# Kernel optimization log

Hardware: AMD Instinct MI355X
Metric: run time of the kernel (lower is better)

The kernel has to match this reference:

```python
import jax, jax.numpy as jnp
import numpy as np

N_NODES = 50000
N_EDGES = 800000
IN_DIM = 1200   # latent_size * num_heads
OUT_DIM = 300
NEG_SLOPE = 0.2  # PyG GATConv default


def setup_inputs() -> dict:
    key = jax.random.key(0)
    k1, k2, k3, k4, k5 = jax.random.split(key, 5)
    z = jax.random.normal(k1, (N_NODES, IN_DIM), dtype=jnp.float32)
    edge_index = jax.random.randint(k2, (2, N_EDGES), 0, N_NODES, dtype=jnp.int64)
    # GATConv params (heads=1): lin weight [out, in], attention vectors [out], bias [out]
    W = jax.random.normal(k3, (OUT_DIM, IN_DIM), dtype=jnp.float32) * (1.0 / np.sqrt(IN_DIM))
    att_src = jax.random.normal(k4, (OUT_DIM,), dtype=jnp.float32) * 0.1
    att_dst = jax.random.normal(k5, (OUT_DIM,), dtype=jnp.float32) * 0.1
    bias = jnp.zeros((OUT_DIM,), dtype=jnp.float32)
    return {"z": z, "edge_index": edge_index, "W": W,
            "att_src": att_src, "att_dst": att_dst, "bias": bias}


def reference(z, edge_index, W, att_src, att_dst, bias):
    N = z.shape[0]
    # Linear projection (no bias on lin in GATConv; bias added after aggregation)
    x = z @ W.T                                   # [N, OUT_DIM]
    # add self-loops (GATConv default add_self_loops=True)
    loop = jnp.arange(N, dtype=edge_index.dtype)
    src = jnp.concatenate([edge_index[0], loop])  # message source j
    dst = jnp.concatenate([edge_index[1], loop])  # message target i
    # per-node attention logits
    a_src = x @ att_src                           # [N]
    a_dst = x @ att_dst                           # [N]
    # per-edge score, softmax over incoming edges of each target node
    e = jax.nn.leaky_relu(a_src[src] + a_dst[dst], negative_slope=NEG_SLOPE)  # [E+N]
    e_max = jax.ops.segment_max(e, dst, num_segments=N)   # every node has a self-loop
    ex = jnp.exp(e - e_max[dst])
    denom = jax.ops.segment_sum(ex, dst, num_segments=N)
    alpha = ex / denom[dst]                       # [E+N]
    # weighted aggregation (scatter-add over targets)
    out = jax.ops.segment_sum(alpha[:, None] * x[src], dst, num_segments=N)
    return out + bias
```

## Files before the change

### kernel.cpp

```cpp
#include <hip/hip_runtime.h>

#define N_NODES 50000
#define N_EDGES 800000
#define IN_DIM  1200
#define OUT_DIM 300
#define XBS     304
#define NSLOTS  (N_EDGES + N_NODES)

typedef __attribute__((ext_vector_type(8))) short short8;
typedef __attribute__((ext_vector_type(4))) float f32x4;

__device__ __forceinline__ short f2bf(float f) {
  unsigned u = __builtin_bit_cast(unsigned, f);
  u += 0x7fffu + ((u >> 16) & 1u);
  return (short)(u >> 16);
}
__device__ __forceinline__ float bf2f(unsigned short h) {
  return __builtin_bit_cast(float, (unsigned)h << 16);
}
__device__ __forceinline__ float lrelu(float v) { return v > 0.f ? v : 0.2f * v; }

__device__ __forceinline__ float wredMaxF(float v) {
  #pragma unroll
  for (int o = 32; o > 0; o >>= 1) v = fmaxf(v, __shfl_xor(v, o));
  return v;
}
__device__ __forceinline__ float wredSumF(float v) {
  #pragma unroll
  for (int o = 32; o > 0; o >>= 1) v += __shfl_xor(v, o);
  return v;
}

__global__ __launch_bounds__(256) void wconv(const float* __restrict__ W,
                                             unsigned short* __restrict__ Wb) {
  int f = blockIdx.x * 256 + threadIdx.x;
  if (f >= 304 * IN_DIM / 8) return;
  int n = (f * 8) / IN_DIM, c = (f * 8) % IN_DIM;
  short8 v = {0,0,0,0,0,0,0,0};
  if (n < OUT_DIM) {
    const float4* p = reinterpret_cast<const float4*>(W + (size_t)n * IN_DIM + c);
    float4 f0 = p[0], f1 = p[1];
    v[0]=f2bf(f0.x); v[1]=f2bf(f0.y); v[2]=f2bf(f0.z); v[3]=f2bf(f0.w);
    v[4]=f2bf(f1.x); v[5]=f2bf(f1.y); v[6]=f2bf(f1.z); v[7]=f2bf(f1.w);
  }
  *reinterpret_cast<short8*>(&Wb[(size_t)n * IN_DIM + c]) = v;
}

__global__ __launch_bounds__(256, 2) void gemm_x(const float* __restrict__ z,
                                                 const unsigned short* __restrict__ Wb,
                                                 const float* __restrict__ att_s,
                                                 const float* __restrict__ att_d,
                                                 unsigned short* __restrict__ xb,
                                                 float* __restrict__ a_s,
                                                 float* __restrict__ a_d) {
  __shared__ unsigned short As[128 * 40];
  __shared__ unsigned short Bs[304 * 40];

  const int tid  = threadIdx.x;
  const int lane = tid & 63;
  const int wid  = tid >> 6;
  const int m0   = blockIdx.x * 128;
  const int lr   = lane & 15;
  const int lg   = lane >> 4;
  const int lk   = lg * 8;

  f32x4 zero4 = {0.f, 0.f, 0.f, 0.f};
  f32x4 acc[2][19];
  #pragma unroll
  for (int h = 0; h < 2; ++h)
    #pragma unroll
    for (int t = 0; t < 19; ++t) acc[h][t] = zero4;

  const int ar = tid >> 1;
  const int ac = (tid & 1) * 16;
  const int bn = tid >> 2;
  const int bc = (tid & 3) * 8;

  for (int kt = 0; kt < 38; ++kt) {
    const int k0 = kt * 32;
    {
      int m = m0 + ar, k = k0 + ac;
      short8 v0 = {0,0,0,0,0,0,0,0}, v1 = v0;
      if (m < N_NODES && k + 15 < IN_DIM) {
        const float4* p = reinterpret_cast<const float4*>(z + (size_t)m * IN_DIM + k);
        float4 f0 = p[0], f1 = p[1], f2 = p[2], f3 = p[3];
        v0[0]=f2bf(f0.x); v0[1]=f2bf(f0.y); v0[2]=f2bf(f0.z); v0[3]=f2bf(f0.w);
        v0[4]=f2bf(f1.x); v0[5]=f2bf(f1.y); v0[6]=f2bf(f1.z); v0[7]=f2bf(f1.w);
        v1[0]=f2bf(f2.x); v1[1]=f2bf(f2.y); v1[2]=f2bf(f2.z); v1[3]=f2bf(f2.w);
        v1[4]=f2bf(f3.x); v1[5]=f2bf(f3.y); v1[6]=f2bf(f3.z); v1[7]=f2bf(f3.w);
      }
      *reinterpret_cast<short8*>(&As[ar * 40 + ac]) = v0;
      *reinterpret_cast<short8*>(&As[ar * 40 + ac + 8]) = v1;
    }
    #pragma unroll
    for (int p5 = 0; p5 < 5; ++p5) {
      int n = bn + 64 * p5;
      if (n < 304) {
        int k = k0 + bc;
        short8 v = {0,0,0,0,0,0,0,0};
        if (k + 7 < IN_DIM)
          v = *reinterpret_cast<const short8*>(&Wb[(size_t)n * IN_DIM + k]);
        *reinterpret_cast<short8*>(&Bs[n * 40 + bc]) = v;
      }
    }
    __syncthreads();

    short8 af0 = *reinterpret_cast<const short8*>(&As[(32 * wid + lr) * 40 + lk]);
    short8 af1 = *reinterpret_cast<const short8*>(&As[(32 * wid + 16 + lr) * 40 + lk]);
    #pragma unroll
    for (int t = 0; t < 19; ++t) {
      short8 bf = *reinterpret_cast<const short8*>(&Bs[(16 * t + lr) * 40 + lk]);
      acc[0][t] = __builtin_amdgcn_mfma_f32_16x16x32_bf16(af0, bf, acc[0][t], 0, 0, 0);
      acc[1][t] = __builtin_amdgcn_mfma_f32_16x16x32_bf16(af1, bf, acc[1][t], 0, 0, 0);
    }
    __syncthreads();
  }

  #pragma unroll
  for (int h = 0; h < 2; ++h) {
    const int rbase = m0 + 32 * wid + 16 * h + 4 * lg;
    float ps[4] = {0.f,0.f,0.f,0.f}, pd[4] = {0.f,0.f,0.f,0.f};
    #pragma unroll
    for (int t = 0; t < 19; ++t) {
      int c = 16 * t + lr;
      if (c < OUT_DIM) {
        float vs = att_s[c], vd = att_d[c];
        #pragma unroll
        for (int j = 0; j < 4; ++j) {
          float val = acc[h][t][j];
          int r = rbase + j;
          if (r < N_NODES) xb[(size_t)r * XBS + c] = (unsigned short)f2bf(val);
          ps[j] += val * vs;
          pd[j] += val * vd;
        }
      }
    }
    #pragma unroll
    for (int j = 0; j < 4; ++j) {
      #pragma unroll
      for (int o = 8; o > 0; o >>= 1) {
        ps[j] += __shfl_xor(ps[j], o);
        pd[j] += __shfl_xor(pd[j], o);
      }
    }
    if (lr == 0) {
      #pragma unroll
      for (int j = 0; j < 4; ++j) {
        int r = rbase + j;
        if (r < N_NODES) { a_s[r] = ps[j]; a_d[r] = pd[j]; }
      }
    }
  }
}

__global__ void hist(const int* __restrict__ ei, int* __restrict__ deg) {
  int e = blockIdx.x * blockDim.x + threadIdx.x;
  if (e < N_EDGES) {
    unsigned dst = (unsigned)ei[N_EDGES + e];
    if (dst < N_NODES) atomicAdd(&deg[dst], 1);
  }
}

#define SCAN_B 1024
#define NBLK   49

__global__ __launch_bounds__(SCAN_B) void scan1(const int* __restrict__ deg,
                                                int* __restrict__ bsum) {
  int i = blockIdx.x * SCAN_B + threadIdx.x;
  int v = (i < N_NODES) ? deg[i] + 1 : 0;
  #pragma unroll
  for (int o = 32; o > 0; o >>= 1) v += __shfl_xor(v, o);
  __shared__ int wt[16];
  if ((threadIdx.x & 63) == 0) wt[threadIdx.x >> 6] = v;
  __syncthreads();
  if (threadIdx.x == 0) {
    int t = 0;
    #pragma unroll
    for (int w = 0; w < 16; ++w) t += wt[w];
    bsum[blockIdx.x] = t;
  }
}

__global__ void scan2(const int* __restrict__ bsum, int* __restrict__ bex,
                      int* __restrict__ offs) {
  int l = threadIdx.x;
  int v = (l < NBLK) ? bsum[l] : 0;
  int incl = v;
  #pragma unroll
  for (int off = 1; off < 64; off <<= 1) {
    int u = __shfl_up(incl, off);
    if (l >= off) incl += u;
  }
  if (l < NBLK) bex[l] = incl - v;
  if (l == NBLK - 1) offs[N_NODES] = incl;
}

__global__ __launch_bounds__(SCAN_B) void scan3(const int* __restrict__ deg,
                                                const int* __restrict__ bex,
                                                int* __restrict__ offs,
                                                int* __restrict__ cursor) {
  int tid = threadIdx.x;
  int i = blockIdx.x * SCAN_B + tid;
  int lane = tid & 63, wid = tid >> 6;
  int v = (i < N_NODES) ? deg[i] + 1 : 0;
  int incl = v;
  #pragma unroll
  for (int off = 1; off < 64; off <<= 1) {
    int u = __shfl_up(incl, off);
    if (lane >= off) incl += u;
  }
  __shared__ int wt[16];
  if (lane == 63) wt[wid] = incl;
  __syncthreads();
  if (tid < 16) {
    int t = wt[tid];
    int sc = t;
    #pragma unroll
    for (int off = 1; off < 16; off <<= 1) {
      int u = __shfl_up(sc, off);
      if (tid >= off) sc += u;
    }
    wt[tid] = sc - t;
  }
  __syncthreads();
  int excl = incl - v + wt[wid] + bex[blockIdx.x];
  if (i < N_NODES) { offs[i] = excl; cursor[i] = excl; }
}

__global__ void fill(const int* __restrict__ ei, int* __restrict__ cursor,
                     int* __restrict__ srcs) {
  int e = blockIdx.x * blockDim.x + threadIdx.x;
  if (e < N_EDGES) {
    unsigned dst = (unsigned)ei[N_EDGES + e];
    unsigned src = (unsigned)ei[e];
    if (dst < N_NODES && src < N_NODES) {
      int pos = atomicAdd(&cursor[dst], 1);
      srcs[pos] = (int)src;
    }
  }
}

__global__ __launch_bounds__(256) void weights(const float* __restrict__ a_s,
                                               const float* __restrict__ a_d,
                                               const int* __restrict__ offs,
                                               const int* __restrict__ srcs,
                                               int2* __restrict__ packed) {
  int node = blockIdx.x * 4 + (threadIdx.x >> 6);
  if (node >= N_NODES) return;
  int lane = threadIdx.x & 63;
  int beg = offs[node], end = offs[node + 1];
  int ne = end - 1 - beg;
  float adi = a_d[node];
  float eself = lrelu(a_s[node] + adi);

  float m = eself;
  for (int k = lane; k < ne; k += 64)
    m = fmaxf(m, lrelu(a_s[srcs[beg + k]] + adi));
  m = wredMaxF(m);

  float s = 0.f;
  for (int k = lane; k < ne; k += 64)
    s += expf(lrelu(a_s[srcs[beg + k]] + adi) - m);
  s = wredSumF(s) + expf(eself - m);
  float inv = 1.0f / s;

  for (int k = lane; k < ne; k += 64) {
    int sj = srcs[beg + k];
    float w = expf(lrelu(a_s[sj] + adi) - m) * inv;
    packed[beg + k] = make_int2(sj, __float_as_int(w));
  }
  if (lane == 0)
    packed[end - 1] = make_int2(node, __float_as_int(expf(eself - m) * inv));
}

__global__ __launch_bounds__(256) void aggregate(const unsigned short* __restrict__ xb,
                                                 const int2* __restrict__ packed,
                                                 const int* __restrict__ offs,
                                                 const float* __restrict__ bias,
                                                 float* __restrict__ out) {
  unsigned wi = blockIdx.x * 256u + threadIdx.x;
  if (wi >= (unsigned)N_NODES * 75u) return;
  unsigned node = wi / 75u;
  unsigned cc = wi - node * 75u;

  int beg = offs[node], end = offs[node + 1];
  const unsigned short* xcol = xb + 4u * cc;

  float4 acc = {0.f, 0.f, 0.f, 0.f};
  for (int k = beg; k < end; ++k) {
    int2 pw = packed[k];
    float w = __builtin_bit_cast(float, pw.y);
    ushort4 xv = *reinterpret_cast<const ushort4*>(xcol + (size_t)pw.x * XBS);
    acc.x += w * bf2f(xv.x);
    acc.y += w * bf2f(xv.y);
    acc.z += w * bf2f(xv.z);
    acc.w += w * bf2f(xv.w);
  }
  const float4 b = *reinterpret_cast<const float4*>(bias + 4u * cc);
  float4 o = {acc.x + b.x, acc.y + b.y, acc.z + b.z, acc.w + b.w};
  *reinterpret_cast<float4*>(out + (size_t)node * OUT_DIM + 4u * cc) = o;
}

extern "C" void kernel_launch(void* const* d_in, const int* in_sizes, int n_in,
                              void* d_out, int out_size, void* d_ws, size_t ws_size,
                              hipStream_t stream) {
  const float* z     = (const float*)d_in[0];
  const int*   ei    = (const int*)d_in[1];
  const float* W     = (const float*)d_in[2];
  const float* att_s = (const float*)d_in[3];
  const float* att_d = (const float*)d_in[4];
  const float* bias  = (const float*)d_in[5];
  float* out = (float*)d_out;

  char* ws = (char*)d_ws;
  size_t off = 0;
  unsigned short* xb   = (unsigned short*)(ws + off); off += (size_t)N_NODES * XBS * 2;
  unsigned short* Wb   = (unsigned short*)(ws + off); off += (size_t)304 * IN_DIM * 2;
  float* a_s  = (float*)(ws + off); off += 50048 * 4;
  float* a_d  = (float*)(ws + off); off += 50048 * 4;
  int*   deg  = (int*)(ws + off);   off += 50048 * 4;
  int*   offs = (int*)(ws + off);   off += 50056 * 4;
  int*   cur  = (int*)(ws + off);   off += 50048 * 4;
  int*   bsum = (int*)(ws + off);   off += 64 * 4;
  int*   bex  = (int*)(ws + off);   off += 64 * 4;
  int*   srcs = (int*)(ws + off);   off += (size_t)NSLOTS * 4;
  int2*  pck  = (int2*)(ws + off);  off += (size_t)NSLOTS * 8;

  hipMemsetAsync(deg, 0, N_NODES * 4, stream);

  wconv<<<(304 * IN_DIM / 8 + 255) / 256, 256, 0, stream>>>(W, Wb);
  gemm_x<<<(N_NODES + 127) / 128, 256, 0, stream>>>(z, Wb, att_s, att_d, xb, a_s, a_d);
  hist<<<(N_EDGES + 255) / 256, 256, 0, stream>>>(ei, deg);
  scan1<<<NBLK, SCAN_B, 0, stream>>>(deg, bsum);
  scan2<<<1, 64, 0, stream>>>(bsum, bex, offs);
  scan3<<<NBLK, SCAN_B, 0, stream>>>(deg, bex, offs, cur);
  fill<<<(N_EDGES + 255) / 256, 256, 0, stream>>>(ei, cur, srcs);
  weights<<<(N_NODES + 3) / 4, 256, 0, stream>>>(a_s, a_d, offs, srcs, pck);
  aggregate<<<((unsigned)N_NODES * 75u + 255) / 256, 256, 0, stream>>>(xb, pck, offs, bias, out);
}
```

Baseline: 364.3 us.

## Restructure projection GEMM tiling and widen per-thread aggregation columns

The projection GEMM moves from 128-row tiles with both operands staged in LDS to 96-row tiles. Only z is staged in LDS, with an XOR swizzle and register prefetch of the next K-tile. Each wave reads its 80-column slice of padded bf16 W directly from global memory, and the attention-logit reduction now goes across waves through LDS. The aggregate kernel gives each thread 20 columns instead of 4, so each thread reads the packed edge entry once per 20 columns instead of once per 4. The cost is higher register pressure and fewer threads, which lowers the parallelism available to hide gather latency.

```diff
diff --git a/kernel.cpp b/kernel.cpp
--- a/kernel.cpp
+++ b/kernel.cpp
@@ -3,9 +3,13 @@
 #define N_NODES 50000
 #define N_EDGES 800000
 #define IN_DIM  1200
+#define KP      1216
 #define OUT_DIM 300
+#define BNP     320
 #define XBS     304
 #define NSLOTS  (N_EDGES + N_NODES)
+#define BM      96
+#define GRID_M  ((N_NODES + BM - 1) / BM)
 
 typedef __attribute__((ext_vector_type(8))) short short8;
 typedef __attribute__((ext_vector_type(4))) float f32x4;
@@ -34,16 +38,16 @@
 __global__ __launch_bounds__(256) void wconv(const float* __restrict__ W,
                                              unsigned short* __restrict__ Wb) {
   int f = blockIdx.x * 256 + threadIdx.x;
-  if (f >= 304 * IN_DIM / 8) return;
-  int n = (f * 8) / IN_DIM, c = (f * 8) % IN_DIM;
+  if (f >= BNP * KP / 8) return;
+  int n = (f * 8) / KP, c = (f * 8) % KP;
   short8 v = {0,0,0,0,0,0,0,0};
-  if (n < OUT_DIM) {
+  if (n < OUT_DIM && c < IN_DIM) {
     const float4* p = reinterpret_cast<const float4*>(W + (size_t)n * IN_DIM + c);
     float4 f0 = p[0], f1 = p[1];
     v[0]=f2bf(f0.x); v[1]=f2bf(f0.y); v[2]=f2bf(f0.z); v[3]=f2bf(f0.w);
     v[4]=f2bf(f1.x); v[5]=f2bf(f1.y); v[6]=f2bf(f1.z); v[7]=f2bf(f1.w);
   }
-  *reinterpret_cast<short8*>(&Wb[(size_t)n * IN_DIM + c]) = v;
+  *reinterpret_cast<short8*>(&Wb[(size_t)n * KP + c]) = v;
 }
 
 __global__ __launch_bounds__(256, 2) void gemm_x(const float* __restrict__ z,
@@ -53,103 +57,131 @@
                                                  unsigned short* __restrict__ xb,
                                                  float* __restrict__ a_s,
                                                  float* __restrict__ a_d) {
-  __shared__ unsigned short As[128 * 40];
-  __shared__ unsigned short Bs[304 * 40];
+  __shared__ unsigned short As[BM * 64];
 
   const int tid  = threadIdx.x;
   const int lane = tid & 63;
   const int wid  = tid >> 6;
-  const int m0   = blockIdx.x * 128;
   const int lr   = lane & 15;
   const int lg   = lane >> 4;
-  const int lk   = lg * 8;
+  const int m0   = blockIdx.x * BM;
 
   f32x4 zero4 = {0.f, 0.f, 0.f, 0.f};
-  f32x4 acc[2][19];
-  #pragma unroll
-  for (int h = 0; h < 2; ++h)
-    #pragma unroll
-    for (int t = 0; t < 19; ++t) acc[h][t] = zero4;
-
-  const int ar = tid >> 1;
-  const int ac = (tid & 1) * 16;
-  const int bn = tid >> 2;
-  const int bc = (tid & 3) * 8;
-
-  for (int kt = 0; kt < 38; ++kt) {
-    const int k0 = kt * 32;
-    {
-      int m = m0 + ar, k = k0 + ac;
-      short8 v0 = {0,0,0,0,0,0,0,0}, v1 = v0;
-      if (m < N_NODES && k + 15 < IN_DIM) {
-        const float4* p = reinterpret_cast<const float4*>(z + (size_t)m * IN_DIM + k);
-        float4 f0 = p[0], f1 = p[1], f2 = p[2], f3 = p[3];
-        v0[0]=f2bf(f0.x); v0[1]=f2bf(f0.y); v0[2]=f2bf(f0.z); v0[3]=f2bf(f0.w);
-        v0[4]=f2bf(f1.x); v0[5]=f2bf(f1.y); v0[6]=f2bf(f1.z); v0[7]=f2bf(f1.w);
-        v1[0]=f2bf(f2.x); v1[1]=f2bf(f2.y); v1[2]=f2bf(f2.z); v1[3]=f2bf(f2.w);
-        v1[4]=f2bf(f3.x); v1[5]=f2bf(f3.y); v1[6]=f2bf(f3.z); v1[7]=f2bf(f3.w);
+  const float4 fz4 = make_float4(0.f, 0.f, 0.f, 0.f);
+  f32x4 acc[6][5];
+  #pragma unroll
+  for (int mf = 0; mf < 6; ++mf)
+    #pragma unroll
+    for (int nj = 0; nj < 5; ++nj) acc[mf][nj] = zero4;
+
+  const unsigned short* bp = Wb + (size_t)(80 * wid + lr) * KP + lg * 8;
+
+  float4 st[3][2];
+  const int srow[3] = { (tid + 0)   >> 3, (tid + 256) >> 3, (tid + 512) >> 3 };
+  const int sch [3] = { (tid + 0)   & 7,  (tid + 256) & 7,  (tid + 512) & 7  };
+
+  #define LOADST(KT)                                                          \
+    _Pragma("unroll")                                                         \
+    for (int j = 0; j < 3; ++j) {                                             \
+      int m = m0 + srow[j], k = (KT) * 64 + sch[j] * 8;                       \
+      if (m < N_NODES && k < IN_DIM) {                                        \
+        const float4* p = reinterpret_cast<const float4*>(z + (size_t)m * IN_DIM + k); \
+        st[j][0] = p[0]; st[j][1] = p[1];                                     \
+      } else { st[j][0] = fz4; st[j][1] = fz4; }                              \
+    }
+
+  LOADST(0);
+
+  for (int kt = 0; kt < 19; ++kt) {
+    __syncthreads();
+    #pragma unroll
+    for (int j = 0; j < 3; ++j) {
+      short8 v;
+      v[0]=f2bf(st[j][0].x); v[1]=f2bf(st[j][0].y); v[2]=f2bf(st[j][0].z); v[3]=f2bf(st[j][0].w);
+      v[4]=f2bf(st[j][1].x); v[5]=f2bf(st[j][1].y); v[6]=f2bf(st[j][1].z); v[7]=f2bf(st[j][1].w);
+      int c2 = sch[j] ^ (srow[j] & 7);
+      *reinterpret_cast<short8*>(&As[srow[j] * 64 + c2 * 8]) = v;
+    }
+    __syncthreads();
+    if (kt < 18) { LOADST(kt + 1) }
+
+    const unsigned short* bpk = bp + kt * 64;
+    short8 bfr[5][2];
+    #pragma unroll
+    for (int nj = 0; nj < 5; ++nj) {
+      bfr[nj][0] = *reinterpret_cast<const short8*>(bpk + (size_t)nj * 16 * KP);
+      bfr[nj][1] = *reinterpret_cast<const short8*>(bpk + (size_t)nj * 16 * KP + 32);
+    }
+
+    const int sw = lr & 7;
+    #pragma unroll
+    for (int mf = 0; mf < 6; ++mf) {
+      int arow = mf * 16 + lr;
+      short8 a0 = *reinterpret_cast<const short8*>(&As[arow * 64 + ((lg    ) ^ sw) * 8]);
+      short8 a1 = *reinterpret_cast<const short8*>(&As[arow * 64 + ((4 + lg) ^ sw) * 8]);
+      #pragma unroll
+      for (int nj = 0; nj < 5; ++nj) {
+        acc[mf][nj] = __builtin_amdgcn_mfma_f32_16x16x32_bf16(a0, bfr[nj][0], acc[mf][nj], 0, 0, 0);
+        acc[mf][nj] = __builtin_amdgcn_mfma_f32_16x16x32_bf16(a1, bfr[nj][1], acc[mf][nj], 0, 0, 0);
       }
-      *reinterpret_cast<short8*>(&As[ar * 40 + ac]) = v0;
-      *reinterpret_cast<short8*>(&As[ar * 40 + ac + 8]) = v1;
-    }
-    #pragma unroll
-    for (int p5 = 0; p5 < 5; ++p5) {
-      int n = bn + 64 * p5;
-      if (n < 304) {
-        int k = k0 + bc;
-        short8 v = {0,0,0,0,0,0,0,0};
-        if (k + 7 < IN_DIM)
-          v = *reinterpret_cast<const short8*>(&Wb[(size_t)n * IN_DIM + k]);
-        *reinterpret_cast<short8*>(&Bs[n * 40 + bc]) = v;
+    }
+  }
+  #undef LOADST
+
+  __syncthreads();
+  float* red = reinterpret_cast<float*>(As);
+
+  float vs[5], vd[5];
+  #pragma unroll
+  for (int nj = 0; nj < 5; ++nj) {
+    int c = 80 * wid + 16 * nj + lr;
+    bool cv = c < OUT_DIM;
+    vs[nj] = cv ? att_s[c] : 0.f;
+    vd[nj] = cv ? att_d[c] : 0.f;
+  }
+
+  #pragma unroll
+  for (int mf = 0; mf < 6; ++mf) {
+    float ps[4] = {0.f,0.f,0.f,0.f}, pd[4] = {0.f,0.f,0.f,0.f};
+    #pragma unroll
+    for (int nj = 0; nj < 5; ++nj) {
+      int c = 80 * wid + 16 * nj + lr;
+      bool cv = c < OUT_DIM;
+      #pragma unroll
+      for (int jj = 0; jj < 4; ++jj) {
+        float val = acc[mf][nj][jj];
+        int r = m0 + 16 * mf + 4 * lg + jj;
+        if (cv && r < N_NODES) xb[(size_t)r * XBS + c] = (unsigned short)f2bf(val);
+        ps[jj] += val * vs[nj];
+        pd[jj] += val * vd[nj];
       }
     }
-    __syncthreads();
-
-    short8 af0 = *reinterpret_cast<const short8*>(&As[(32 * wid + lr) * 40 + lk]);
-    short8 af1 = *reinterpret_cast<const short8*>(&As[(32 * wid + 16 + lr) * 40 + lk]);
-    #pragma unroll
-    for (int t = 0; t < 19; ++t) {
-      short8 bf = *reinterpret_cast<const short8*>(&Bs[(16 * t + lr) * 40 + lk]);
-      acc[0][t] = __builtin_amdgcn_mfma_f32_16x16x32_bf16(af0, bf, acc[0][t], 0, 0, 0);
-      acc[1][t] = __builtin_amdgcn_mfma_f32_16x16x32_bf16(af1, bf, acc[1][t], 0, 0, 0);
-    }
-    __syncthreads();
-  }
-
-  #pragma unroll
-  for (int h = 0; h < 2; ++h) {
-    const int rbase = m0 + 32 * wid + 16 * h + 4 * lg;
-    float ps[4] = {0.f,0.f,0.f,0.f}, pd[4] = {0.f,0.f,0.f,0.f};
-    #pragma unroll
-    for (int t = 0; t < 19; ++t) {
-      int c = 16 * t + lr;
-      if (c < OUT_DIM) {
-        float vs = att_s[c], vd = att_d[c];
-        #pragma unroll
-        for (int j = 0; j < 4; ++j) {
-          float val = acc[h][t][j];
-          int r = rbase + j;
-          if (r < N_NODES) xb[(size_t)r * XBS + c] = (unsigned short)f2bf(val);
-          ps[j] += val * vs;
-          pd[j] += val * vd;
-        }
-      }
-    }
-    #pragma unroll
-    for (int j = 0; j < 4; ++j) {
+    #pragma unroll
+    for (int jj = 0; jj < 4; ++jj) {
       #pragma unroll
       for (int o = 8; o > 0; o >>= 1) {
-        ps[j] += __shfl_xor(ps[j], o);
-        pd[j] += __shfl_xor(pd[j], o);
+        ps[jj] += __shfl_xor(ps[jj], o);
+        pd[jj] += __shfl_xor(pd[jj], o);
       }
     }
     if (lr == 0) {
       #pragma unroll
-      for (int j = 0; j < 4; ++j) {
-        int r = rbase + j;
-        if (r < N_NODES) { a_s[r] = ps[j]; a_d[r] = pd[j]; }
+      for (int jj = 0; jj < 4; ++jj) {
+        int rr = 16 * mf + 4 * lg + jj;
+        red[wid * 96 + rr]       = ps[jj];
+        red[384 + wid * 96 + rr] = pd[jj];
       }
     }
+  }
+  __syncthreads();
+  if (tid < 96) {
+    int r = m0 + tid;
+    if (r < N_NODES)
+      a_s[r] = red[tid] + red[96 + tid] + red[192 + tid] + red[288 + tid];
+  } else if (tid < 192) {
+    int t = tid - 96, r = m0 + t;
+    if (r < N_NODES)
+      a_d[r] = red[384 + t] + red[384 + 96 + t] + red[384 + 192 + t] + red[384 + 288 + t];
   }
 }
 
@@ -273,32 +305,45 @@
     packed[end - 1] = make_int2(node, __float_as_int(expf(eself - m) * inv));
 }
 
+#define CCH 15
 __global__ __launch_bounds__(256) void aggregate(const unsigned short* __restrict__ xb,
                                                  const int2* __restrict__ packed,
                                                  const int* __restrict__ offs,
                                                  const float* __restrict__ bias,
                                                  float* __restrict__ out) {
   unsigned wi = blockIdx.x * 256u + threadIdx.x;
-  if (wi >= (unsigned)N_NODES * 75u) return;
-  unsigned node = wi / 75u;
-  unsigned cc = wi - node * 75u;
+  if (wi >= (unsigned)N_NODES * CCH) return;
+  unsigned node = wi / CCH;
+  unsigned cc = wi - node * CCH;
 
   int beg = offs[node], end = offs[node + 1];
-  const unsigned short* xcol = xb + 4u * cc;
-
-  float4 acc = {0.f, 0.f, 0.f, 0.f};
+  const unsigned short* xcol = xb + 20u * cc;
+
+  float acc[20];
+  #pragma unroll
+  for (int q = 0; q < 20; ++q) acc[q] = 0.f;
+
   for (int k = beg; k < end; ++k) {
     int2 pw = packed[k];
     float w = __builtin_bit_cast(float, pw.y);
-    ushort4 xv = *reinterpret_cast<const ushort4*>(xcol + (size_t)pw.x * XBS);
-    acc.x += w * bf2f(xv.x);
-    acc.y += w * bf2f(xv.y);
-    acc.z += w * bf2f(xv.z);
-    acc.w += w * bf2f(xv.w);
-  }
-  const float4 b = *reinterpret_cast<const float4*>(bias + 4u * cc);
-  float4 o = {acc.x + b.x, acc.y + b.y, acc.z + b.z, acc.w + b.w};
-  *reinterpret_cast<float4*>(out + (size_t)node * OUT_DIM + 4u * cc) = o;
+    const unsigned short* xr = xcol + (size_t)pw.x * XBS;
+    #pragma unroll
+    for (int q = 0; q < 5; ++q) {
+      ushort4 xv = *reinterpret_cast<const ushort4*>(xr + 4 * q);
+      acc[4*q+0] += w * bf2f(xv.x);
+      acc[4*q+1] += w * bf2f(xv.y);
+      acc[4*q+2] += w * bf2f(xv.z);
+      acc[4*q+3] += w * bf2f(xv.w);
+    }
+  }
+  float* op = out + (size_t)node * OUT_DIM + 20u * cc;
+  const float* bp = bias + 20u * cc;
+  #pragma unroll
+  for (int q = 0; q < 5; ++q) {
+    float4 b = *reinterpret_cast<const float4*>(bp + 4 * q);
+    float4 o = {acc[4*q] + b.x, acc[4*q+1] + b.y, acc[4*q+2] + b.z, acc[4*q+3] + b.w};
+    *reinterpret_cast<float4*>(op + 4 * q) = o;
+  }
 }
 
 extern "C" void kernel_launch(void* const* d_in, const int* in_sizes, int n_in,
@@ -314,8 +359,8 @@
 
   char* ws = (char*)d_ws;
   size_t off = 0;
-  unsigned short* xb   = (unsigned short*)(ws + off); off += (size_t)N_NODES * XBS * 2;
-  unsigned short* Wb   = (unsigned short*)(ws + off); off += (size_t)304 * IN_DIM * 2;
+  unsigned short* xb = (unsigned short*)(ws + off); off += (size_t)N_NODES * XBS * 2;
+  unsigned short* Wb = (unsigned short*)(ws + off); off += (size_t)BNP * KP * 2;
   float* a_s  = (float*)(ws + off); off += 50048 * 4;
   float* a_d  = (float*)(ws + off); off += 50048 * 4;
   int*   deg  = (int*)(ws + off);   off += 50048 * 4;
@@ -326,15 +371,15 @@
   int*   srcs = (int*)(ws + off);   off += (size_t)NSLOTS * 4;
   int2*  pck  = (int2*)(ws + off);  off += (size_t)NSLOTS * 8;
 
-  hipMemsetAsync(deg, 0, N_NODES * 4, stream);
-
-  wconv<<<(304 * IN_DIM / 8 + 255) / 256, 256, 0, stream>>>(W, Wb);
-  gemm_x<<<(N_NODES + 127) / 128, 256, 0, stream>>>(z, Wb, att_s, att_d, xb, a_s, a_d);
+  (void)hipMemsetAsync(deg, 0, N_NODES * 4, stream);
+
+  wconv<<<(BNP * KP / 8 + 255) / 256, 256, 0, stream>>>(W, Wb);
+  gemm_x<<<GRID_M, 256, 0, stream>>>(z, Wb, att_s, att_d, xb, a_s, a_d);
   hist<<<(N_EDGES + 255) / 256, 256, 0, stream>>>(ei, deg);
   scan1<<<NBLK, SCAN_B, 0, stream>>>(deg, bsum);
   scan2<<<1, 64, 0, stream>>>(bsum, bex, offs);
   scan3<<<NBLK, SCAN_B, 0, stream>>>(deg, bex, offs, cur);
   fill<<<(N_EDGES + 255) / 256, 256, 0, stream>>>(ei, cur, srcs);
   weights<<<(N_NODES + 3) / 4, 256, 0, stream>>>(a_s, a_d, offs, srcs, pck);
-  aggregate<<<((unsigned)N_NODES * 75u + 255) / 256, 256, 0, stream>>>(xb, pck, offs, bias, out);
-}
+  aggregate<<<((unsigned)N_NODES * CCH + 255) / 256, 256, 0, stream>>>(xb, pck, offs, bias, out);
+}
```

Measured after the change: 363.6 us. No clear change (-0.2%).
